# Optimization experiments

Measured on AMD Instinct MI355X. Metric: run time of the kernel, lower is better.

## Reference

```python
import jax, jax.numpy as jnp
import numpy as np

MARGIN = 0.2

def setup_inputs() -> dict:
    key = jax.random.key(0)
    kx, ky = jax.random.split(key)
    N, D = 8192, 128
    x = jax.random.normal(kx, (N, D), dtype=jnp.float32)
    y = jax.random.normal(ky, (N, D), dtype=jnp.float32)
    return {"x": x, "y": y}

def reference(x, y):
    N = x.shape[0]
    # pairwise squared distances: [N, N]
    xx = jnp.sum(x * x, axis=1)[:, None]
    yy = jnp.sum(y * y, axis=1)[None, :]
    pdist = xx + yy - 2.0 * (x @ y.T)
    d_pos = jnp.diagonal(pdist)  # [N]
    # non-hardest branch: loss = relu(d_pos - pdist + margin), diag zeroed, mean over N*N
    loss = jnp.maximum(d_pos[:, None] - pdist + MARGIN, 0.0)
    off_diag = ~jnp.eye(N, dtype=bool)
    loss = jnp.where(off_diag, loss, 0.0)
    return jnp.mean(loss)
```

## Files before the change

### kernel.cpp

```cpp
#include <hip/hip_runtime.h>
#include <hip/hip_bf16.h>

typedef __bf16 bf16x8 __attribute__((ext_vector_type(8)));
typedef float f32x4 __attribute__((ext_vector_type(4)));

#define DDIM 128
#define TM 128
#define JCOLS 512
#define MARGIN_F 0.2f

__global__ __launch_bounds__(256)
void prep_v5_kernel(const float* __restrict__ x, const float* __restrict__ y,
                    __bf16* __restrict__ xb, __bf16* __restrict__ yb,
                    float* __restrict__ yy, float* __restrict__ crow,
                    float* __restrict__ out, float out_init)
{
    const int t   = threadIdx.x;
    const int row = blockIdx.x * 16 + (t >> 4);
    const int c   = t & 15;
    const float* xr = x + (size_t)row * DDIM + c * 8;
    const float* yr = y + (size_t)row * DDIM + c * 8;
    const float4 xa = *(const float4*)xr;
    const float4 xc = *(const float4*)(xr + 4);
    const float4 ya = *(const float4*)yr;
    const float4 yc = *(const float4*)(yr + 4);
    bf16x8 xv, yv;
    xv[0]=(__bf16)(2.0f*xa.x); xv[1]=(__bf16)(2.0f*xa.y); xv[2]=(__bf16)(2.0f*xa.z); xv[3]=(__bf16)(2.0f*xa.w);
    xv[4]=(__bf16)(2.0f*xc.x); xv[5]=(__bf16)(2.0f*xc.y); xv[6]=(__bf16)(2.0f*xc.z); xv[7]=(__bf16)(2.0f*xc.w);
    yv[0]=(__bf16)ya.x; yv[1]=(__bf16)ya.y; yv[2]=(__bf16)ya.z; yv[3]=(__bf16)ya.w;
    yv[4]=(__bf16)yc.x; yv[5]=(__bf16)yc.y; yv[6]=(__bf16)yc.z; yv[7]=(__bf16)yc.w;
    const int dst = ((row >> 4) * 4 + (c >> 2)) * 64 + (c & 3) * 16 + (row & 15);
    ((bf16x8*)xb)[dst] = xv;
    ((bf16x8*)yb)[dst] = yv;

    float sy  = ya.x*ya.x + ya.y*ya.y + ya.z*ya.z + ya.w*ya.w
              + yc.x*yc.x + yc.y*yc.y + yc.z*yc.z + yc.w*yc.w;
    float sxy = xa.x*ya.x + xa.y*ya.y + xa.z*ya.z + xa.w*ya.w
              + xc.x*yc.x + xc.y*yc.y + xc.z*yc.z + xc.w*yc.w;
    #pragma unroll
    for (int o = 8; o; o >>= 1) {
        sy  += __shfl_xor(sy,  o);
        sxy += __shfl_xor(sxy, o);
    }
    if (c == 0) {
        yy[row]   = sy;
        crow[row] = sy - 2.0f * sxy + MARGIN_F;
    }
    if (t == 0 && blockIdx.x == 0) out[0] = out_init;
}

__global__ __launch_bounds__(256, 3)
void triplet_v5_kernel(const __bf16* __restrict__ xb, const __bf16* __restrict__ yb,
                       const float* __restrict__ yy, const float* __restrict__ crow,
                       float* __restrict__ out, float inv_n2)
{
    __shared__ float wsum[4];
    const int t    = threadIdx.x;
    const int w    = t >> 6;
    const int lane = t & 63;
    const int l4   = lane >> 4;
    const int l15  = lane & 15;
    const int wm   = w >> 1;
    const int wn   = w & 1;
    const int jg     = blockIdx.x;
    const int istrip = blockIdx.y;

    bf16x8 af[4][4];
    {
        const bf16x8* ap = (const bf16x8*)xb + ((size_t)(istrip * 8 + wm * 4) * 4) * 64 + lane;
        #pragma unroll
        for (int mi = 0; mi < 4; ++mi)
            #pragma unroll
            for (int kk = 0; kk < 4; ++kk)
                af[kk][mi] = ap[(mi * 4 + kk) * 64];
    }
    const int rlo = istrip * TM + wm * 64;
    float ctv[16];
    #pragma unroll
    for (int mi = 0; mi < 4; ++mi) {
        const float4 c4 = *(const float4*)&crow[rlo + mi * 16 + l4 * 4];
        ctv[mi*4+0] = c4.x; ctv[mi*4+1] = c4.y; ctv[mi*4+2] = c4.z; ctv[mi*4+3] = c4.w;
    }
    const int cb0 = jg * 32 + wn * 16;
    float yyv[16];
    #pragma unroll
    for (int s = 0; s < 16; ++s)
        yyv[s] = yy[(cb0 + s) * 16 + l15];

    float lsum[4] = {0.0f, 0.0f, 0.0f, 0.0f};

    const bf16x8* bp0 = (const bf16x8*)yb + ((size_t)cb0 * 4) * 64 + lane;
    #pragma unroll
    for (int s = 0; s < 16; ++s) {
        const bf16x8* bp = bp0 + (size_t)s * 256;
        bf16x8 bfv[4];
        #pragma unroll
        for (int kk = 0; kk < 4; ++kk) bfv[kk] = bp[kk * 64];

        f32x4 acc[4] = {};
        #pragma unroll
        for (int kk = 0; kk < 4; ++kk)
            #pragma unroll
            for (int mi = 0; mi < 4; ++mi)
                acc[mi] = __builtin_amdgcn_mfma_f32_16x16x32_bf16(
                    af[kk][mi], bfv[kk], acc[mi], 0, 0, 0);

        #pragma unroll
        for (int mi = 0; mi < 4; ++mi) {
            #pragma unroll
            for (int r = 0; r < 4; ++r)
                lsum[r] += fmaxf(acc[mi][r] + (ctv[mi*4+r] - yyv[s]), 0.0f);
        }
    }

    float ls = (lsum[0] + lsum[1]) + (lsum[2] + lsum[3]);
    #pragma unroll
    for (int off = 32; off; off >>= 1) ls += __shfl_xor(ls, off);
    if (lane == 0) wsum[w] = ls;
    __syncthreads();
    if (t == 0)
        atomicAdd(out, (wsum[0] + wsum[1] + wsum[2] + wsum[3]) * inv_n2);
}


#define TILE 128
#define LDSK 136

__global__ __launch_bounds__(256)
void prep_f32_kernel(const float* __restrict__ x, const float* __restrict__ y,
                     float* __restrict__ yy, float* __restrict__ crow,
                     float* __restrict__ out)
{
    const int t    = threadIdx.x;
    const int lane = t & 63;
    const int row  = blockIdx.x * 4 + (t >> 6);
    const float2 xv = ((const float2*)(x + (size_t)row * DDIM))[lane];
    const float2 yv = ((const float2*)(y + (size_t)row * DDIM))[lane];
    float sy  = yv.x * yv.x + yv.y * yv.y;
    float sxy = xv.x * yv.x + xv.y * yv.y;
    #pragma unroll
    for (int off = 32; off; off >>= 1) {
        sy  += __shfl_xor(sy,  off);
        sxy += __shfl_xor(sxy, off);
    }
    if (lane == 0) { yy[row] = sy; crow[row] = sy - 2.0f * sxy; }
    if (t == 0 && blockIdx.x == 0) out[0] = 0.0f;
}

__global__ __launch_bounds__(256)
void triplet_f32_kernel(const float* __restrict__ x, const float* __restrict__ y,
                        const float* __restrict__ yy, const float* __restrict__ crow,
                        float* __restrict__ out, float inv_n2)
{
    __shared__ __bf16 As[TILE][LDSK];
    __shared__ __bf16 Bs[TILE][LDSK];
    __shared__ float ctile[TILE];
    __shared__ float yytile[TILE];
    __shared__ float wsum[4];

    const int t  = threadIdx.x;
    const int bi = blockIdx.y;
    const int bj = blockIdx.x;
    {
        const int rr = t >> 4;
        const int cc = (t & 15) * 8;
        const float* xp = x + (size_t)bi * TILE * DDIM;
        const float* yp = y + (size_t)bj * TILE * DDIM;
        #pragma unroll
        for (int it = 0; it < 8; ++it) {
            const int r = it * 16 + rr;
            const float4 a0 = *(const float4*)(xp + (size_t)r * DDIM + cc);
            const float4 a1 = *(const float4*)(xp + (size_t)r * DDIM + cc + 4);
            bf16x8 av;
            av[0] = (__bf16)a0.x; av[1] = (__bf16)a0.y; av[2] = (__bf16)a0.z; av[3] = (__bf16)a0.w;
            av[4] = (__bf16)a1.x; av[5] = (__bf16)a1.y; av[6] = (__bf16)a1.z; av[7] = (__bf16)a1.w;
            *(bf16x8*)&As[r][cc] = av;
            const float4 b0 = *(const float4*)(yp + (size_t)r * DDIM + cc);
            const float4 b1 = *(const float4*)(yp + (size_t)r * DDIM + cc + 4);
            bf16x8 bv;
            bv[0] = (__bf16)b0.x; bv[1] = (__bf16)b0.y; bv[2] = (__bf16)b0.z; bv[3] = (__bf16)b0.w;
            bv[4] = (__bf16)b1.x; bv[5] = (__bf16)b1.y; bv[6] = (__bf16)b1.z; bv[7] = (__bf16)b1.w;
            *(bf16x8*)&Bs[r][cc] = bv;
        }
        if (t < TILE) ctile[t]         = crow[bi * TILE + t];
        else          yytile[t - TILE] = yy[bj * TILE + (t - TILE)];
    }
    __syncthreads();

    const int wave = t >> 6;
    const int lane = t & 63;
    const int wm   = wave >> 1;
    const int wn   = wave & 1;
    const int l4   = lane >> 4;
    const int l15  = lane & 15;

    f32x4 acc[4][4] = {};
    #pragma unroll
    for (int kk = 0; kk < 4; ++kk) {
        const int kb = kk * 32 + l4 * 8;
        bf16x8 af[4], bfv[4];
        #pragma unroll
        for (int mi = 0; mi < 4; ++mi) af[mi] = *(const bf16x8*)&As[wm * 64 + mi * 16 + l15][kb];
        #pragma unroll
        for (int ni = 0; ni < 4; ++ni) bfv[ni] = *(const bf16x8*)&Bs[wn * 64 + ni * 16 + l15][kb];
        #pragma unroll
        for (int mi = 0; mi < 4; ++mi)
            #pragma unroll
            for (int ni = 0; ni < 4; ++ni)
                acc[mi][ni] = __builtin_amdgcn_mfma_f32_16x16x32_bf16(af[mi], bfv[ni], acc[mi][ni], 0, 0, 0);
    }

    float lsum = 0.0f;
    #pragma unroll
    for (int ni = 0; ni < 4; ++ni) {
        const int ct    = wn * 64 + ni * 16 + l15;
        const float yyv = yytile[ct];
        const int gj    = bj * TILE + ct;
        #pragma unroll
        for (int mi = 0; mi < 4; ++mi)
            #pragma unroll
            for (int r = 0; r < 4; ++r) {
                const int rt = wm * 64 + mi * 16 + l4 * 4 + r;
                float v = fmaxf(2.0f * acc[mi][ni][r] + ctile[rt] - yyv + MARGIN_F, 0.0f);
                if (bi * TILE + rt == gj) v = 0.0f;
                lsum += v;
            }
    }
    #pragma unroll
    for (int off = 32; off; off >>= 1) lsum += __shfl_xor(lsum, off);
    if (lane == 0) wsum[wave] = lsum;
    __syncthreads();
    if (t == 0) atomicAdd(out, (wsum[0] + wsum[1] + wsum[2] + wsum[3]) * inv_n2);
}


extern "C" void kernel_launch(void* const* d_in, const int* in_sizes, int n_in,
                              void* d_out, int out_size, void* d_ws, size_t ws_size,
                              hipStream_t stream)
{
    const float* x = (const float*)d_in[0];
    const float* y = (const float*)d_in[1];
    float* out = (float*)d_out;
    const int N = in_sizes[0] / DDIM;
    const float inv_n2 = 1.0f / ((float)N * (float)N);

    const size_t bf_bytes = (size_t)N * DDIM * sizeof(__bf16);
    const size_t need = 2 * bf_bytes + 2 * (size_t)N * sizeof(float);

    if (ws_size >= need && (N % JCOLS) == 0) {
        __bf16* xb  = (__bf16*)d_ws;
        __bf16* yb  = xb + (size_t)N * DDIM;
        float*  yy  = (float*)(yb + (size_t)N * DDIM);
        float*  crw = yy + N;
        const float out_init = -MARGIN_F / (float)N;
        prep_v5_kernel<<<dim3(N / 16), dim3(256), 0, stream>>>(x, y, xb, yb, yy, crw, out, out_init);
        triplet_v5_kernel<<<dim3(N / JCOLS, N / TM), dim3(256), 0, stream>>>(
            xb, yb, yy, crw, out, inv_n2);
    } else {
        float* yy  = (float*)d_ws;
        float* crw = yy + N;
        prep_f32_kernel<<<dim3(N / 4), dim3(256), 0, stream>>>(x, y, yy, crw, out);
        triplet_f32_kernel<<<dim3(N / TILE, N / TILE), dim3(256), 0, stream>>>(
            x, y, yy, crw, out, inv_n2);
    }
}
```

Baseline: 80.78 us.

## Switch pairwise dot products to FP8 MFMA with partial-sum reduction kernel

Quantizes x and y to FP8 (e4m3) in the prep kernel instead of bf16 and uses the 16x16x32 fp8 MFMA, halving operand bytes and fragment registers so occupancy can rise to four blocks per CU. The epilogue uses packed two-wide float ops, and per-block sums go to a partials buffer reduced by a separate single-block kernel instead of atomics. FP8 loses substantial precision on the dot products, which risks loss accuracy versus the reference, and adds an extra kernel launch.

```diff
diff --git a/kernel.cpp b/kernel.cpp
--- a/kernel.cpp
+++ b/kernel.cpp
@@ -1,8 +1,9 @@
 #include <hip/hip_runtime.h>
 #include <hip/hip_bf16.h>
 
-typedef __bf16 bf16x8 __attribute__((ext_vector_type(8)));
 typedef float f32x4 __attribute__((ext_vector_type(4)));
+typedef float f32x2 __attribute__((ext_vector_type(2)));
+typedef long  i64;
 
 #define DDIM 128
 #define TM 128
@@ -10,10 +11,9 @@
 #define MARGIN_F 0.2f
 
 __global__ __launch_bounds__(256)
-void prep_v5_kernel(const float* __restrict__ x, const float* __restrict__ y,
-                    __bf16* __restrict__ xb, __bf16* __restrict__ yb,
-                    float* __restrict__ yy, float* __restrict__ crow,
-                    float* __restrict__ out, float out_init)
+void prep_v6_kernel(const float* __restrict__ x, const float* __restrict__ y,
+                    char* __restrict__ xq, char* __restrict__ yq,
+                    float* __restrict__ yy, float* __restrict__ crow)
 {
     const int t   = threadIdx.x;
     const int row = blockIdx.x * 16 + (t >> 4);
@@ -24,14 +24,23 @@
     const float4 xc = *(const float4*)(xr + 4);
     const float4 ya = *(const float4*)yr;
     const float4 yc = *(const float4*)(yr + 4);
-    bf16x8 xv, yv;
-    xv[0]=(__bf16)(2.0f*xa.x); xv[1]=(__bf16)(2.0f*xa.y); xv[2]=(__bf16)(2.0f*xa.z); xv[3]=(__bf16)(2.0f*xa.w);
-    xv[4]=(__bf16)(2.0f*xc.x); xv[5]=(__bf16)(2.0f*xc.y); xv[6]=(__bf16)(2.0f*xc.z); xv[7]=(__bf16)(2.0f*xc.w);
-    yv[0]=(__bf16)ya.x; yv[1]=(__bf16)ya.y; yv[2]=(__bf16)ya.z; yv[3]=(__bf16)ya.w;
-    yv[4]=(__bf16)yc.x; yv[5]=(__bf16)yc.y; yv[6]=(__bf16)yc.z; yv[7]=(__bf16)yc.w;
-    const int dst = ((row >> 4) * 4 + (c >> 2)) * 64 + (c & 3) * 16 + (row & 15);
-    ((bf16x8*)xb)[dst] = xv;
-    ((bf16x8*)yb)[dst] = yv;
+
+    int x01 = __builtin_amdgcn_cvt_pk_fp8_f32(2.0f*xa.x, 2.0f*xa.y, 0, false);
+    int x23 = __builtin_amdgcn_cvt_pk_fp8_f32(2.0f*xa.z, 2.0f*xa.w, 0, false);
+    int x45 = __builtin_amdgcn_cvt_pk_fp8_f32(2.0f*xc.x, 2.0f*xc.y, 0, false);
+    int x67 = __builtin_amdgcn_cvt_pk_fp8_f32(2.0f*xc.z, 2.0f*xc.w, 0, false);
+    int y01 = __builtin_amdgcn_cvt_pk_fp8_f32(ya.x, ya.y, 0, false);
+    int y23 = __builtin_amdgcn_cvt_pk_fp8_f32(ya.z, ya.w, 0, false);
+    int y45 = __builtin_amdgcn_cvt_pk_fp8_f32(yc.x, yc.y, 0, false);
+    int y67 = __builtin_amdgcn_cvt_pk_fp8_f32(yc.z, yc.w, 0, false);
+    int2 xp, yp;
+    xp.x = (x01 & 0xffff) | (x23 << 16);  xp.y = (x45 & 0xffff) | (x67 << 16);
+    yp.x = (y01 & 0xffff) | (y23 << 16);  yp.y = (y45 & 0xffff) | (y67 << 16);
+
+    const size_t base = (size_t)(row >> 4) * 2048 + (size_t)((c >> 3)) * 1024
+                      + (size_t)((c & 3) * 16 + (row & 15)) * 16 + (size_t)(((c >> 2) & 1)) * 8;
+    *(int2*)(xq + base) = xp;
+    *(int2*)(yq + base) = yp;
 
     float sy  = ya.x*ya.x + ya.y*ya.y + ya.z*ya.z + ya.w*ya.w
               + yc.x*yc.x + yc.y*yc.y + yc.z*yc.z + yc.w*yc.w;
@@ -46,13 +55,12 @@
         yy[row]   = sy;
         crow[row] = sy - 2.0f * sxy + MARGIN_F;
     }
-    if (t == 0 && blockIdx.x == 0) out[0] = out_init;
-}
-
-__global__ __launch_bounds__(256, 3)
-void triplet_v5_kernel(const __bf16* __restrict__ xb, const __bf16* __restrict__ yb,
+}
+
+__global__ __launch_bounds__(256, 4)
+void triplet_v6_kernel(const char* __restrict__ xq, const char* __restrict__ yq,
                        const float* __restrict__ yy, const float* __restrict__ crow,
-                       float* __restrict__ out, float inv_n2)
+                       float* __restrict__ partials)
 {
     __shared__ float wsum[4];
     const int t    = threadIdx.x;
@@ -65,66 +73,87 @@
     const int jg     = blockIdx.x;
     const int istrip = blockIdx.y;
 
-    bf16x8 af[4][4];
+    i64 af[4][4];
     {
-        const bf16x8* ap = (const bf16x8*)xb + ((size_t)(istrip * 8 + wm * 4) * 4) * 64 + lane;
+        const char* ap = xq + (size_t)(istrip * 8 + wm * 4) * 2048 + (size_t)lane * 16;
         #pragma unroll
         for (int mi = 0; mi < 4; ++mi)
             #pragma unroll
-            for (int kk = 0; kk < 4; ++kk)
-                af[kk][mi] = ap[(mi * 4 + kk) * 64];
+            for (int kk2 = 0; kk2 < 2; ++kk2) {
+                const long2 q = *(const long2*)(ap + mi * 2048 + kk2 * 1024);
+                af[2*kk2][mi]     = q.x;
+                af[2*kk2 + 1][mi] = q.y;
+            }
     }
     const int rlo = istrip * TM + wm * 64;
-    float ctv[16];
+    f32x2 ctv[8];
     #pragma unroll
     for (int mi = 0; mi < 4; ++mi) {
         const float4 c4 = *(const float4*)&crow[rlo + mi * 16 + l4 * 4];
-        ctv[mi*4+0] = c4.x; ctv[mi*4+1] = c4.y; ctv[mi*4+2] = c4.z; ctv[mi*4+3] = c4.w;
-    }
+        ctv[mi*2+0] = (f32x2){c4.x, c4.y};
+        ctv[mi*2+1] = (f32x2){c4.z, c4.w};
+    }
+
     const int cb0 = jg * 32 + wn * 16;
-    float yyv[16];
-    #pragma unroll
-    for (int s = 0; s < 16; ++s)
-        yyv[s] = yy[(cb0 + s) * 16 + l15];
-
-    float lsum[4] = {0.0f, 0.0f, 0.0f, 0.0f};
-
-    const bf16x8* bp0 = (const bf16x8*)yb + ((size_t)cb0 * 4) * 64 + lane;
+    f32x2 lsum2[2] = {(f32x2){0.f,0.f}, (f32x2){0.f,0.f}};
+
     #pragma unroll
     for (int s = 0; s < 16; ++s) {
-        const bf16x8* bp = bp0 + (size_t)s * 256;
-        bf16x8 bfv[4];
-        #pragma unroll
-        for (int kk = 0; kk < 4; ++kk) bfv[kk] = bp[kk * 64];
+        const char* bp = yq + (size_t)(cb0 + s) * 2048 + (size_t)lane * 16;
+        const long2 q0 = *(const long2*)(bp);
+        const long2 q1 = *(const long2*)(bp + 1024);
+        i64 bfv[4] = {q0.x, q0.y, q1.x, q1.y};
+        const float yyv = yy[(cb0 + s) * 16 + l15];
 
         f32x4 acc[4] = {};
         #pragma unroll
         for (int kk = 0; kk < 4; ++kk)
             #pragma unroll
             for (int mi = 0; mi < 4; ++mi)
-                acc[mi] = __builtin_amdgcn_mfma_f32_16x16x32_bf16(
+                acc[mi] = __builtin_amdgcn_mfma_f32_16x16x32_fp8_fp8(
                     af[kk][mi], bfv[kk], acc[mi], 0, 0, 0);
 
+        const f32x2 yy2 = (f32x2){yyv, yyv};
         #pragma unroll
         for (int mi = 0; mi < 4; ++mi) {
             #pragma unroll
-            for (int r = 0; r < 4; ++r)
-                lsum[r] += fmaxf(acc[mi][r] + (ctv[mi*4+r] - yyv[s]), 0.0f);
+            for (int rp = 0; rp < 2; ++rp) {
+                f32x2 a = (f32x2){acc[mi][2*rp], acc[mi][2*rp+1]};
+                a = a + (ctv[mi*2+rp] - yy2);
+                lsum2[rp] += __builtin_elementwise_max(a, (f32x2){0.f, 0.f});
+            }
         }
     }
 
-    float ls = (lsum[0] + lsum[1]) + (lsum[2] + lsum[3]);
+    float ls = (lsum2[0][0] + lsum2[0][1]) + (lsum2[1][0] + lsum2[1][1]);
     #pragma unroll
     for (int off = 32; off; off >>= 1) ls += __shfl_xor(ls, off);
     if (lane == 0) wsum[w] = ls;
     __syncthreads();
     if (t == 0)
-        atomicAdd(out, (wsum[0] + wsum[1] + wsum[2] + wsum[3]) * inv_n2);
+        partials[blockIdx.y * gridDim.x + blockIdx.x] =
+            (wsum[0] + wsum[1]) + (wsum[2] + wsum[3]);
+}
+
+__global__ __launch_bounds__(256)
+void reduce_v6_kernel(const float* __restrict__ partials, float* __restrict__ out,
+                      float inv_n2, float diag_corr)
+{
+    __shared__ float wsum[4];
+    const int t = threadIdx.x;
+    float s = partials[t] + partials[t + 256] + partials[t + 512] + partials[t + 768];
+    #pragma unroll
+    for (int off = 32; off; off >>= 1) s += __shfl_xor(s, off);
+    if ((t & 63) == 0) wsum[t >> 6] = s;
+    __syncthreads();
+    if (t == 0)
+        out[0] = ((wsum[0] + wsum[1]) + (wsum[2] + wsum[3])) * inv_n2 + diag_corr;
 }
 
 
 #define TILE 128
 #define LDSK 136
+typedef __bf16 bf16x8 __attribute__((ext_vector_type(8)));
 
 __global__ __launch_bounds__(256)
 void prep_f32_kernel(const float* __restrict__ x, const float* __restrict__ y,
@@ -244,18 +273,20 @@
     const int N = in_sizes[0] / DDIM;
     const float inv_n2 = 1.0f / ((float)N * (float)N);
 
-    const size_t bf_bytes = (size_t)N * DDIM * sizeof(__bf16);
-    const size_t need = 2 * bf_bytes + 2 * (size_t)N * sizeof(float);
+    const size_t q_bytes = (size_t)N * DDIM;
+    const size_t need = 2 * q_bytes + 2 * (size_t)N * sizeof(float) + 4096 * sizeof(float);
 
     if (ws_size >= need && (N % JCOLS) == 0) {
-        __bf16* xb  = (__bf16*)d_ws;
-        __bf16* yb  = xb + (size_t)N * DDIM;
-        float*  yy  = (float*)(yb + (size_t)N * DDIM);
-        float*  crw = yy + N;
-        const float out_init = -MARGIN_F / (float)N;
-        prep_v5_kernel<<<dim3(N / 16), dim3(256), 0, stream>>>(x, y, xb, yb, yy, crw, out, out_init);
-        triplet_v5_kernel<<<dim3(N / JCOLS, N / TM), dim3(256), 0, stream>>>(
-            xb, yb, yy, crw, out, inv_n2);
+        char*  xq  = (char*)d_ws;
+        char*  yq  = xq + q_bytes;
+        float* yy  = (float*)(yq + q_bytes);
+        float* crw = yy + N;
+        float* par = crw + N;
+        const float diag_corr = -MARGIN_F / (float)N;
+        prep_v6_kernel<<<dim3(N / 16), dim3(256), 0, stream>>>(x, y, xq, yq, yy, crw);
+        triplet_v6_kernel<<<dim3(N / JCOLS, N / TM), dim3(256), 0, stream>>>(
+            xq, yq, yy, crw, par);
+        reduce_v6_kernel<<<dim3(1), dim3(256), 0, stream>>>(par, out, inv_n2, diag_corr);
     } else {
         float* yy  = (float*)d_ws;
         float* crw = yy + N;
```

Result: faster. 76.89 us (-4.8%).
